# Optimization experiments

Measured on AMD Instinct MI355X. Metric: run time of the kernel, lower is better.

The kernel has to match this reference:

```python
import jax, jax.numpy as jnp
import numpy as np
from jax import lax

BLANK = 0
LOGZERO = -1e30  # finite stand-in for -inf (keeps grads NaN-free, exact in fp32 logaddexp)


def setup_inputs() -> dict:
    key = jax.random.key(0)
    k1, k2 = jax.random.split(key)
    T, B, V, S = 512, 32, 4096, 128
    logits = jax.random.normal(k1, (T, B, V), dtype=jnp.float32)
    log_probs = jax.nn.log_softmax(logits, axis=-1)
    targets = jax.random.randint(k2, (B, S), 1, V, dtype=jnp.int32)  # avoid blank label
    input_lengths = jnp.full((B,), T, dtype=jnp.int32)   # must be >= 2*S+1
    target_lengths = jnp.full((B,), S, dtype=jnp.int32)
    return {"log_probs": log_probs, "targets": targets,
            "input_lengths": input_lengths, "target_lengths": target_lengths}


def _shift_right(a, n):
    # a: (B, L) log-space; shift states right by n, filling with log(0)
    pad = jnp.full(a.shape[:-1] + (n,), LOGZERO, dtype=a.dtype)
    return jnp.concatenate([pad, a[..., :-n]], axis=-1)


def _ctc_log_likelihood(log_probs, targets, input_lengths, target_lengths):
    # Vectorized CTC forward (alpha) recursion over the blank-interleaved trellis.
    # Mathematically identical to the per-sample bounded DP in the torch module:
    # states outside the reachability bounds carry log(0) / never feed the terminal sum.
    T, B, V = log_probs.shape
    S = targets.shape[1]
    L = 2 * S + 1
    blanked = jnp.full((B, L), BLANK, dtype=jnp.int32).at[:, 1::2].set(targets)
    # emission log-prob of each trellis state at each time: (T, B, L)
    emit = jnp.take_along_axis(log_probs, jnp.broadcast_to(blanked[None], (T, B, L)), axis=2)
    idx = jnp.arange(L)
    # skip transition (j-2 -> j) allowed for label states whose label differs from previous label
    skip = (idx % 2 == 1) & (idx >= 2) & (blanked != jnp.roll(blanked, 2, axis=1))  # (B, L)

    alpha0 = jnp.full((B, L), LOGZERO, dtype=log_probs.dtype)
    alpha0 = alpha0.at[:, 0].set(emit[0, :, 0]).at[:, 1].set(emit[0, :, 1])

    def step(alpha, xs):
        emit_t, t = xs  # emit_t: (B, L)
        pre = jnp.logaddexp(alpha, _shift_right(alpha, 1))
        pre = jnp.where(skip, jnp.logaddexp(pre, _shift_right(alpha, 2)), pre)
        new = emit_t + pre
        new = jnp.where((t < input_lengths)[:, None], new, alpha)  # freeze past each sample's length
        return new, None

    alpha, _ = lax.scan(step, alpha0, (emit[1:], jnp.arange(1, T)))
    b = jnp.arange(B)
    end = 2 * target_lengths  # final blank state index per sample
    ll = jnp.logaddexp(alpha[b, end], alpha[b, end - 1])  # log p(target | input)
    return ll


def reference(log_probs, targets, input_lengths, target_lengths):
    ll = _ctc_log_likelihood(log_probs, targets, input_lengths, target_lengths)
    B = log_probs.shape[1]
    # faithful to the module's 'mean' branch: (ret / target_lengths / B).sum()  (NOT negated)
    return (ll / target_lengths.astype(ll.dtype) / B).sum()
```

## Files before the change

### kernel.cpp

```cpp
#include <hip/hip_runtime.h>
#include <hip/hip_bf16.h>
#include <cstdint>

typedef unsigned short u16;
typedef uint32_t u32;

constexpr int Tc = 512, Bc = 32, Vc = 4096, Sc = 128;
constexpr int BOOST = 13;
constexpr int DPF = 16;
constexpr float LOG2E = 1.4426950408889634f;
constexpr float LN2 = 0.6931471805599453f;

__device__ __forceinline__ float bflo(u32 p) { return __uint_as_float(p << 16); }
__device__ __forceinline__ float bfhi(u32 p) { return __uint_as_float(p & 0xffff0000u); }

__device__ __forceinline__ u16 f2bf(float f) {
    __hip_bfloat16 h = __float2bfloat16(f);
    return *reinterpret_cast<u16*>(&h);
}

__global__ __launch_bounds__(256) void k_gather(const float* __restrict__ lp,
                                                const int* __restrict__ tgt,
                                                u16* __restrict__ emitT,
                                                float* __restrict__ blankT) {
    __shared__ float row[Vc];
    const int t = blockIdx.x;
    const int b = blockIdx.y;
    const float4* src4 = reinterpret_cast<const float4*>(lp + ((size_t)t * Bc + b) * Vc);
    float4* row4 = reinterpret_cast<float4*>(row);
#pragma unroll
    for (int i = 0; i < Vc / 4 / 256; ++i)
        row4[threadIdx.x + i * 256] = src4[threadIdx.x + i * 256];
    __syncthreads();
    const int s = threadIdx.x;
    if (s < Sc) {
        const int lab = tgt[b * Sc + s];
        const float e = __builtin_amdgcn_exp2f(fmaf(row[lab], LOG2E, (float)BOOST));
        emitT[((size_t)b * Tc + t) * Sc + s] = f2bf(e);
    }
    if (s == 0) {
        blankT[(size_t)b * Tc + t] =
            __builtin_amdgcn_exp2f(fmaf(row[0], LOG2E, (float)BOOST));
    }
}

template <int CTRL, int RMASK>
__device__ __forceinline__ float dppmax(float v) {
    int t = __builtin_amdgcn_update_dpp(__float_as_int(v), __float_as_int(v),
                                        CTRL, RMASK, 0xf, false);
    return fmaxf(v, __int_as_float(t));
}
__device__ __forceinline__ float wave_max_bcast(float v) {
    v = dppmax<0x111, 0xf>(v);
    v = dppmax<0x112, 0xf>(v);
    v = dppmax<0x114, 0xf>(v);
    v = dppmax<0x118, 0xf>(v);
    v = dppmax<0x142, 0xa>(v);
    v = dppmax<0x143, 0xc>(v);
    return __int_as_float(__builtin_amdgcn_readlane(__float_as_int(v), 63));
}

__device__ __forceinline__ float wave_shr1(float v) {
    return __int_as_float(__builtin_amdgcn_update_dpp(
        0, __float_as_int(v), 0x138, 0xf, 0xf, true));
}

__global__ __launch_bounds__(64) void k_ctc(const u16* __restrict__ emitT,
                                            const float* __restrict__ blankT,
                                            const int* __restrict__ tgt,
                                            const int* __restrict__ in_len,
                                            const int* __restrict__ tg_len,
                                            float* __restrict__ out) {
    const int b = blockIdx.x;
    const int lane = threadIdx.x;
    const u32* prow = reinterpret_cast<const u32*>(emitT + (size_t)b * Tc * Sc);
    const float* brow = blankT + (size_t)b * Tc;

    const int tg0 = tgt[b * Sc + 2 * lane];
    const int tg1 = tgt[b * Sc + 2 * lane + 1];
    const int tgm = (lane > 0) ? tgt[b * Sc + 2 * lane - 1] : tg0;
    const float m1 = (lane > 0 && tg0 != tgm) ? 1.f : 0.f;
    const float m3 = (tg1 != tg0) ? 1.f : 0.f;
    const float sel = (lane == 63) ? 1.f : 0.f;

    const int steps = min(in_len[b], Tc) - 1;

    const u32 p0 = prow[lane];
    float a0 = (lane == 0) ? brow[0] : 0.f;
    float a1 = (lane == 0) ? bflo(p0) : 0.f;
    float a2 = 0.f, a3 = 0.f, a4 = 0.f;
    int e_acc = 0;

    u32 pk[DPF];
    float bk[DPF];
#pragma unroll
    for (int d = 0; d < DPF; ++d) {
        pk[d] = prow[(size_t)(1 + d) * 64 + lane];
        bk[d] = brow[1 + d];
    }

#define STEP_N(d) {                                                 \
        const float e1 = bflo(pk[d]);                               \
        const float e3 = bfhi(pk[d]);                               \
        const float ebl = bk[d];                                    \
        pk[d] = prow[(size_t)(t + DPF) * 64 + lane];                \
        bk[d] = brow[t + DPF];                                      \
        const float sh = wave_shr1(a3);                             \
        const float s01 = a0 + a1;                                  \
        const float s12 = a1 + a2;                                  \
        const float s23 = a2 + a3;                                  \
        const float n0 = ebl * (a0 + sh);                           \
        const float n1 = e1 * fmaf(m1, sh, s01);                    \
        const float n3 = e3 * fmaf(m3, a1, s23);                    \
        a4 = ebl * fmaf(sel, a3, a4);                               \
        a0 = n0; a1 = n1; a2 = ebl * s12; a3 = n3;                  \
        ++t; }

#define STEP_T(d) {                                                 \
        const float e1 = bflo(pk[d]);                               \
        const float e3 = bfhi(pk[d]);                               \
        const float ebl = bk[d];                                    \
        const float sh = wave_shr1(a3);                             \
        const float s01 = a0 + a1;                                  \
        const float s12 = a1 + a2;                                  \
        const float s23 = a2 + a3;                                  \
        const float n0 = ebl * (a0 + sh);                           \
        const float n1 = e1 * fmaf(m1, sh, s01);                    \
        const float n2 = ebl * s12;                                 \
        const float n3 = e3 * fmaf(m3, a1, s23);                    \
        const float n4 = ebl * fmaf(sel, a3, a4);                   \
        const bool live = (t <= steps);                             \
        a0 = live ? n0 : a0; a1 = live ? n1 : a1;                   \
        a2 = live ? n2 : a2; a3 = live ? n3 : a3;                   \
        a4 = live ? n4 : a4;                                        \
        ++t; }

#define RENORM() {                                                  \
        float m = fmaxf(fmaxf(fmaxf(a0, a1), fmaxf(a2, a3)), a4);   \
        m = wave_max_bcast(m);                                      \
        int e = (int)((__float_as_uint(m) >> 23) & 0xffu) - 127;    \
        float scale = __uint_as_float((u32)(127 - e) << 23);        \
        a0 *= scale; a1 *= scale; a2 *= scale;                      \
        a3 *= scale; a4 *= scale;                                   \
        e_acc += e; }

    int t = 1;
    const int nfull = steps >> 4;
    for (int g = 0; g < nfull; ++g) {
#pragma unroll
        for (int d = 0; d < 8; ++d) STEP_N(d)
        RENORM()
#pragma unroll
        for (int d = 8; d < 16; ++d) STEP_N(d)
        RENORM()
    }
#pragma unroll
    for (int d = 0; d < 8; ++d) STEP_T(d)
    RENORM()
#pragma unroll
    for (int d = 8; d < 16; ++d) STEP_T(d)
    RENORM()
#undef STEP_N
#undef STEP_T
#undef RENORM

    __shared__ float sa[257];
    sa[4 * lane + 0] = a0;
    sa[4 * lane + 1] = a1;
    sa[4 * lane + 2] = a2;
    sa[4 * lane + 3] = a3;
    if (lane == 63) sa[256] = a4;
    __syncthreads();
    if (lane == 0) {
        const int tl = tg_len[b];
        const int ei = 2 * tl;
        const float ssum = sa[ei] + sa[ei - 1];
        const float ll = __logf(ssum) +
                         LN2 * ((float)e_acc - (float)BOOST * (float)(steps + 1));
        atomicAdd(out, ll / (float)tl / (float)Bc);
    }
}

extern "C" void kernel_launch(void* const* d_in, const int* in_sizes, int n_in,
                              void* d_out, int out_size, void* d_ws, size_t ws_size,
                              hipStream_t stream) {
    const float* lp = (const float*)d_in[0];
    const int* tgt = (const int*)d_in[1];
    const int* in_len = (const int*)d_in[2];
    const int* tg_len = (const int*)d_in[3];

    char* ws = (char*)d_ws;
    float* blankT = (float*)ws;
    u16* emitT = (u16*)(ws + 128 * 1024);

    (void)hipMemsetAsync(d_out, 0, sizeof(float), stream);
    k_gather<<<dim3(Tc, Bc), 256, 0, stream>>>(lp, tgt, emitT, blankT);
    k_ctc<<<Bc, 64, 0, stream>>>(emitT, blankT, tgt, in_len, tg_len, (float*)d_out);
}
```

Before: 379.7 us.

## Gather only 64-byte lines holding target labels and pack blank emission into rows

Adds a prep kernel that finds the distinct 16-float cache lines touched by each sample's labels plus blank. The gather kernel then loads only those lines instead of the full 4096-float vocabulary row, which cuts HBM reads from the full log_probs tensor to roughly 129 lines per (t,b). The blank emission is also interleaved into each 65-word emission row, so the CTC kernel reads one combined stream. This costs an extra kernel launch and indirect, scattered loads, but removes most of the read traffic of the previous full-row copy.

```diff
diff --git a/kernel.cpp b/kernel.cpp
--- a/kernel.cpp
+++ b/kernel.cpp
@@ -8,39 +8,80 @@
 constexpr int Tc = 512, Bc = 32, Vc = 4096, Sc = 128;
 constexpr int BOOST = 13;
 constexpr int DPF = 16;
+constexpr int RSTRIDE = 65;
 constexpr float LOG2E = 1.4426950408889634f;
 constexpr float LN2 = 0.6931471805599453f;
 
 __device__ __forceinline__ float bflo(u32 p) { return __uint_as_float(p << 16); }
 __device__ __forceinline__ float bfhi(u32 p) { return __uint_as_float(p & 0xffff0000u); }
 
-__device__ __forceinline__ u16 f2bf(float f) {
+__device__ __forceinline__ u32 f2bf_bits(float f) {
     __hip_bfloat16 h = __float2bfloat16(f);
-    return *reinterpret_cast<u16*>(&h);
-}
-
-__global__ __launch_bounds__(256) void k_gather(const float* __restrict__ lp,
-                                                const int* __restrict__ tgt,
-                                                u16* __restrict__ emitT,
-                                                float* __restrict__ blankT) {
-    __shared__ float row[Vc];
+    return (u32)(*reinterpret_cast<u16*>(&h));
+}
+
+__global__ __launch_bounds__(128) void k_prep(const int* __restrict__ tgt,
+                                              u16* __restrict__ lines,
+                                              u16* __restrict__ pos,
+                                              int* __restrict__ nl) {
+    __shared__ unsigned bm[8];
+    __shared__ u16 wbase[9];
+    __shared__ u16 rank[256];
+    const int b = blockIdx.x;
+    const int s = threadIdx.x;
+    if (s < 8) bm[s] = 0u;
+    __syncthreads();
+    const int lab = tgt[b * Sc + s];
+    const int ln = lab >> 4;
+    atomicOr(&bm[ln >> 5], 1u << (ln & 31));
+    if (s == 0) atomicOr(&bm[0], 1u);
+    __syncthreads();
+    if (s == 0) {
+        int acc = 0;
+        for (int w = 0; w < 8; ++w) { wbase[w] = (u16)acc; acc += __popc(bm[w]); }
+        wbase[8] = (u16)acc;
+        nl[b] = acc;
+    }
+    __syncthreads();
+    for (int l = s; l < 256; l += 128) {
+        const unsigned w = bm[l >> 5];
+        if (w & (1u << (l & 31))) {
+            const int r = wbase[l >> 5] + __popc(w & ((1u << (l & 31)) - 1u));
+            lines[b * 160 + r] = (u16)l;
+            rank[l] = (u16)r;
+        }
+    }
+    __syncthreads();
+    pos[b * Sc + s] = (u16)(rank[ln] * 16 + (lab & 15));
+}
+
+__global__ __launch_bounds__(256) void k_gather2(const float* __restrict__ lp,
+                                                 const u16* __restrict__ lines,
+                                                 const u16* __restrict__ pos,
+                                                 const int* __restrict__ nl,
+                                                 u32* __restrict__ emitT) {
+    __shared__ __align__(16) float vals[129 * 16];
+    __shared__ u16 lpos[Sc];
     const int t = blockIdx.x;
     const int b = blockIdx.y;
-    const float4* src4 = reinterpret_cast<const float4*>(lp + ((size_t)t * Bc + b) * Vc);
-    float4* row4 = reinterpret_cast<float4*>(row);
-#pragma unroll
-    for (int i = 0; i < Vc / 4 / 256; ++i)
-        row4[threadIdx.x + i * 256] = src4[threadIdx.x + i * 256];
-    __syncthreads();
-    const int s = threadIdx.x;
-    if (s < Sc) {
-        const int lab = tgt[b * Sc + s];
-        const float e = __builtin_amdgcn_exp2f(fmaf(row[lab], LOG2E, (float)BOOST));
-        emitT[((size_t)b * Tc + t) * Sc + s] = f2bf(e);
-    }
-    if (s == 0) {
-        blankT[(size_t)b * Tc + t] =
-            __builtin_amdgcn_exp2f(fmaf(row[0], LOG2E, (float)BOOST));
+    const int n = nl[b];
+    const float* row = lp + ((size_t)t * Bc + b) * Vc;
+    const int tid = threadIdx.x;
+    for (int c = tid; c < n * 4; c += 256) {
+        const int line = (int)lines[b * 160 + (c >> 2)];
+        const float4 v = *reinterpret_cast<const float4*>(row + line * 16 + (c & 3) * 4);
+        *reinterpret_cast<float4*>(&vals[c * 4]) = v;
+    }
+    if (tid < Sc) lpos[tid] = pos[b * Sc + tid];
+    __syncthreads();
+    u32* orow = emitT + ((size_t)b * Tc + t) * RSTRIDE;
+    if (tid < 64) {
+        const float e0 = __builtin_amdgcn_exp2f(fmaf(vals[lpos[2 * tid]], LOG2E, (float)BOOST));
+        const float e1 = __builtin_amdgcn_exp2f(fmaf(vals[lpos[2 * tid + 1]], LOG2E, (float)BOOST));
+        orow[tid] = f2bf_bits(e0) | (f2bf_bits(e1) << 16);
+    } else if (tid == 64) {
+        orow[64] = __float_as_uint(
+            __builtin_amdgcn_exp2f(fmaf(vals[0], LOG2E, (float)BOOST)));
     }
 }
 
@@ -65,16 +106,14 @@
         0, __float_as_int(v), 0x138, 0xf, 0xf, true));
 }
 
-__global__ __launch_bounds__(64) void k_ctc(const u16* __restrict__ emitT,
-                                            const float* __restrict__ blankT,
+__global__ __launch_bounds__(64) void k_ctc(const u32* __restrict__ emitT,
                                             const int* __restrict__ tgt,
                                             const int* __restrict__ in_len,
                                             const int* __restrict__ tg_len,
                                             float* __restrict__ out) {
     const int b = blockIdx.x;
     const int lane = threadIdx.x;
-    const u32* prow = reinterpret_cast<const u32*>(emitT + (size_t)b * Tc * Sc);
-    const float* brow = blankT + (size_t)b * Tc;
+    const u32* p = emitT + (size_t)b * Tc * RSTRIDE;
 
     const int tg0 = tgt[b * Sc + 2 * lane];
     const int tg1 = tgt[b * Sc + 2 * lane + 1];
@@ -85,26 +124,28 @@
 
     const int steps = min(in_len[b], Tc) - 1;
 
-    const u32 p0 = prow[lane];
-    float a0 = (lane == 0) ? brow[0] : 0.f;
+    const u32 p0 = p[lane];
+    float a0 = (lane == 0) ? __uint_as_float(p[64]) : 0.f;
     float a1 = (lane == 0) ? bflo(p0) : 0.f;
     float a2 = 0.f, a3 = 0.f, a4 = 0.f;
     int e_acc = 0;
 
     u32 pk[DPF];
     float bk[DPF];
+    const u32* pr = p + RSTRIDE;
 #pragma unroll
     for (int d = 0; d < DPF; ++d) {
-        pk[d] = prow[(size_t)(1 + d) * 64 + lane];
-        bk[d] = brow[1 + d];
-    }
+        pk[d] = pr[d * RSTRIDE + lane];
+        bk[d] = __uint_as_float(pr[d * RSTRIDE + 64]);
+    }
+    const u32* pg = p + (size_t)(DPF + 1) * RSTRIDE;
 
 #define STEP_N(d) {                                                 \
         const float e1 = bflo(pk[d]);                               \
         const float e3 = bfhi(pk[d]);                               \
         const float ebl = bk[d];                                    \
-        pk[d] = prow[(size_t)(t + DPF) * 64 + lane];                \
-        bk[d] = brow[t + DPF];                                      \
+        pk[d] = pg[(d) * RSTRIDE + lane];                           \
+        bk[d] = __uint_as_float(pg[(d) * RSTRIDE + 64]);            \
         const float sh = wave_shr1(a3);                             \
         const float s01 = a0 + a1;                                  \
         const float s12 = a1 + a2;                                  \
@@ -113,8 +154,7 @@
         const float n1 = e1 * fmaf(m1, sh, s01);                    \
         const float n3 = e3 * fmaf(m3, a1, s23);                    \
         a4 = ebl * fmaf(sel, a3, a4);                               \
-        a0 = n0; a1 = n1; a2 = ebl * s12; a3 = n3;                  \
-        ++t; }
+        a0 = n0; a1 = n1; a2 = ebl * s12; a3 = n3;                  }
 
 #define STEP_T(d) {                                                 \
         const float e1 = bflo(pk[d]);                               \
@@ -144,7 +184,6 @@
         a3 *= scale; a4 *= scale;                                   \
         e_acc += e; }
 
-    int t = 1;
     const int nfull = steps >> 4;
     for (int g = 0; g < nfull; ++g) {
 #pragma unroll
@@ -153,7 +192,9 @@
 #pragma unroll
         for (int d = 8; d < 16; ++d) STEP_N(d)
         RENORM()
-    }
+        pg += DPF * RSTRIDE;
+    }
+    int t = nfull * 16 + 1;
 #pragma unroll
     for (int d = 0; d < 8; ++d) STEP_T(d)
     RENORM()
@@ -190,10 +231,13 @@
     const int* tg_len = (const int*)d_in[3];
 
     char* ws = (char*)d_ws;
-    float* blankT = (float*)ws;
-    u16* emitT = (u16*)(ws + 128 * 1024);
+    int* nl = (int*)ws;
+    u16* lines = (u16*)(ws + 256);
+    u16* pos = (u16*)(ws + 16 * 1024);
+    u32* emitT = (u32*)(ws + 32 * 1024);
 
     (void)hipMemsetAsync(d_out, 0, sizeof(float), stream);
-    k_gather<<<dim3(Tc, Bc), 256, 0, stream>>>(lp, tgt, emitT, blankT);
-    k_ctc<<<Bc, 64, 0, stream>>>(emitT, blankT, tgt, in_len, tg_len, (float*)d_out);
-}
+    k_prep<<<Bc, 128, 0, stream>>>(tgt, lines, pos, nl);
+    k_gather2<<<dim3(Tc, Bc), 256, 0, stream>>>(lp, lines, pos, nl, emitT);
+    k_ctc<<<Bc, 64, 0, stream>>>(emitT, tgt, in_len, tg_len, (float*)d_out);
+}
```

Measured after the change: 373.3 us. About the same (-1.7%).
